# Kernel tuning notes

Hardware: AMD Instinct MI355X
Metric: run time of the kernel (lower is better)

The kernel has to match this reference:

```python
import jax, jax.numpy as jnp
import numpy as np

B, T, D_MODEL, D_STATE = 8, 2048, 1024, 256


def setup_inputs() -> dict:
    key = jax.random.key(0)
    ks = jax.random.split(key, 10)
    def lecun(k, shape):
        fan_in = shape[0]
        return jax.random.normal(k, shape, dtype=jnp.float32) / jnp.sqrt(jnp.float32(fan_in))
    return {
        "x": jax.random.normal(ks[0], (B, T, D_MODEL), dtype=jnp.float32),
        "W_in": lecun(ks[1], (D_MODEL, D_STATE)),
        "b_in": jnp.zeros((D_STATE,), dtype=jnp.float32),
        "W_gate": lecun(ks[2], (D_MODEL, D_MODEL)),
        "b_gate": jnp.zeros((D_MODEL,), dtype=jnp.float32),
        "W_out": lecun(ks[3], (D_MODEL, D_MODEL)),
        "b_out": jnp.zeros((D_MODEL,), dtype=jnp.float32),
        "A": lecun(ks[4], (D_STATE, D_STATE)) * 0.1,  # scaled for recurrence stability
        "Bm": lecun(ks[5], (D_STATE, D_STATE)),
        "C": lecun(ks[6], (D_MODEL, D_STATE)),
        "D": lecun(ks[7], (D_MODEL, D_STATE)),
    }


def reference(x, W_in, b_in, W_gate, b_gate, W_out, b_out, A, Bm, C, D):
    # Input projection to state dim and gating branch (Flax Dense: y = x @ kernel + b)
    u = x @ W_in + b_in                      # [B, T, d_state]
    gate = jax.nn.sigmoid(x @ W_gate + b_gate)  # [B, T, d_model]

    # Linear state-space recurrence: h_t = h_{t-1} @ A + u_t @ Bm
    u_t_first = jnp.swapaxes(u, 0, 1)        # [T, B, d_state]
    h0 = jnp.zeros((x.shape[0], A.shape[0]), dtype=x.dtype)

    def step(h, u_t):
        h = h @ A + u_t @ Bm
        return h, h

    _, hs = jax.lax.scan(step, h0, u_t_first)
    hs = jnp.swapaxes(hs, 0, 1)              # [B, T, d_state]

    # Readout y_t = C h_t + D u_t, gated, then output projection
    y = jnp.einsum('btn,dn->btd', hs, C) + jnp.einsum('btn,dn->btd', u, D)
    y = y * gate
    return y @ W_out + b_out
```

## Files before the change

kernel.cpp:

```cpp
#include <hip/hip_runtime.h>
#include <math.h>

#define NT 16384
#define DM 1024
#define DS 256
#define TSEQ 2048
#define KTAPS 16

typedef __bf16 bf16x8 __attribute__((ext_vector_type(8)));
typedef float f32x4 __attribute__((ext_vector_type(4)));

__device__ __forceinline__ unsigned short f2bf(float f) {
  unsigned int u = __float_as_uint(f);
  return (unsigned short)((u + 0x7FFFu + ((u >> 16) & 1u)) >> 16);
}
__device__ __forceinline__ float bf2f(unsigned short s) {
  return __uint_as_float(((unsigned int)s) << 16);
}

__device__ __forceinline__ void gload16(const void* g, void* l) {
  __builtin_amdgcn_global_load_lds(
      (const __attribute__((address_space(1))) unsigned int*)(unsigned long long)g,
      (__attribute__((address_space(3))) unsigned int*)(unsigned int)(unsigned long long)l,
      16, 0, 0);
}

__device__ __forceinline__ int xcd_swizzle(int orig, int nwg) {
  const int q = nwg >> 3, r = nwg & 7;
  const int xcd = orig & 7, idx = orig >> 3;
  return (xcd < r ? xcd * (q + 1) : r * (q + 1) + (xcd - r) * q) + idx;
}

template<int EPI, bool CONV>
__global__ __launch_bounds__(256)
void gemm128(const unsigned short* __restrict__ A, int lda,
             const unsigned short* __restrict__ Bt, int ldb,
             const float* __restrict__ bias, const float* __restrict__ bias2,
             void* Cout, int ldc, unsigned short* gatep,
             const unsigned short* __restrict__ zp, int K)
{
  __shared__ unsigned short As[3][128 * 32];
  __shared__ unsigned short Bs[3][128 * 32];
  const int tid = threadIdx.x;
  const int wave = tid >> 6, lane = tid & 63;
  const int wr = wave >> 1, wc = wave & 1;
  const int gx = gridDim.x;
  const int wg = xcd_swizzle(blockIdx.y * gx + blockIdx.x, gx * gridDim.y);
  const int row0 = (wg / gx) * 128, col0 = (wg % gx) * 128;
  const int ktiles = K >> 5;
  const int kc = CONV ? blockIdx.z : 0;

  auto stage = [&](int t, int bf) {
    const int kg = CONV ? (kc * 1024 + t * 32) : (t * 32);
    const int tap = CONV ? (kg >> 8) : 0;
    const int kin = CONV ? (kg & 255) : kg;
#pragma unroll
    for (int i = 0; i < 2; ++i) {
      const int ci = tid + i * 256;
      const int row = ci >> 2;
      const int chunk = (ci & 3) ^ ((row >> 1) & 3);
      const unsigned short* src;
      if (CONV) {
        const int r = row0 + row;
        src = ((r & (TSEQ - 1)) >= tap)
            ? A + (size_t)(r - tap) * 512 + 256 + kin + chunk * 8
            : zp + chunk * 8;
      } else {
        src = A + (size_t)(row0 + row) * lda + kin + chunk * 8;
      }
      gload16(src, &As[bf][i * 2048 + tid * 8]);
    }
#pragma unroll
    for (int i = 0; i < 2; ++i) {
      const int ci = tid + i * 256;
      const int row = ci >> 2;
      const int chunk = (ci & 3) ^ ((row >> 1) & 3);
      const unsigned short* src = CONV
          ? Bt + ((size_t)tap << 16) + (size_t)(col0 + row) * 256 + kin + chunk * 8
          : Bt + (size_t)(col0 + row) * ldb + kin + chunk * 8;
      gload16(src, &Bs[bf][i * 2048 + tid * 8]);
    }
  };

  f32x4 acc[4][4];
#pragma unroll
  for (int m = 0; m < 4; ++m)
#pragma unroll
    for (int n = 0; n < 4; ++n)
#pragma unroll
      for (int i = 0; i < 4; ++i) acc[m][n][i] = 0.f;

  const int l15 = lane & 15, lhi = lane >> 4;
  const int cs = (lhi ^ ((l15 >> 1) & 3)) * 8;
  const int aro = (wr * 64 + l15) * 32 + cs;
  const int bro = (wc * 64 + l15) * 32 + cs;

  stage(0, 0);
  stage(1, 1);
  for (int t = 0; t < ktiles; ++t) {
    const int bf = t % 3;
    if (t + 1 < ktiles) {
      asm volatile("s_waitcnt vmcnt(4)" ::: "memory");
    } else {
      asm volatile("s_waitcnt vmcnt(0)" ::: "memory");
    }
    asm volatile("s_barrier" ::: "memory");
    if (t + 2 < ktiles) stage(t + 2, (t + 2) % 3);
    bf16x8 a[4], b[4];
#pragma unroll
    for (int m = 0; m < 4; ++m) a[m] = *(const bf16x8*)(&As[bf][aro + m * 512]);
#pragma unroll
    for (int n = 0; n < 4; ++n) b[n] = *(const bf16x8*)(&Bs[bf][bro + n * 512]);
    __builtin_amdgcn_s_setprio(1);
#pragma unroll
    for (int m = 0; m < 4; ++m)
#pragma unroll
      for (int n = 0; n < 4; ++n)
        acc[m][n] = __builtin_amdgcn_mfma_f32_16x16x32_bf16(a[m], b[n], acc[m][n], 0, 0, 0);
    __builtin_amdgcn_s_setprio(0);
  }

  const int rb = row0 + wr * 64 + lhi * 4;
  const int cb = col0 + wc * 64 + l15;
#pragma unroll
  for (int m = 0; m < 4; ++m) {
#pragma unroll
    for (int n = 0; n < 4; ++n) {
      const int c = cb + n * 16;
#pragma unroll
      for (int i = 0; i < 4; ++i) {
        const size_t r = (size_t)rb + m * 16 + i;
        float v = acc[m][n][i];
        if (EPI == 2) {
          unsigned short* o = (unsigned short*)Cout;
          o[r * ldc + c] = f2bf(v * bf2f(gatep[r * ldc + c]));
        } else if (EPI == 3) {
          ((float*)Cout)[r * ldc + c] = v + bias[c];
        } else if (EPI == 4) {
          if (c < 256) {
            ((unsigned short*)Cout)[r * 512 + 256 + c] = f2bf(v + bias[c]);
          } else {
            gatep[r * 1024 + (c - 256)] = f2bf(1.f / (1.f + __expf(-(v + bias2[c - 256]))));
          }
        } else {
          ((unsigned short*)Cout)[((size_t)kc << 22) + r * 256 + c] = f2bf(v);
        }
      }
    }
  }
}

__global__ __launch_bounds__(256)
void reduce4_k(const unsigned short* __restrict__ PK, unsigned short* __restrict__ HU)
{
  const int i = blockIdx.x * 256 + threadIdx.x;
  const size_t e = (size_t)i * 4;
  const int row = i >> 6, col = (i & 63) * 4;
  float s[4] = {0.f, 0.f, 0.f, 0.f};
#pragma unroll
  for (int kc = 0; kc < 4; ++kc) {
    const ushort4 v = *(const ushort4*)(PK + ((size_t)kc << 22) + e);
    s[0] += bf2f(v.x); s[1] += bf2f(v.y); s[2] += bf2f(v.z); s[3] += bf2f(v.w);
  }
  ushort4 o;
  o.x = f2bf(s[0]); o.y = f2bf(s[1]); o.z = f2bf(s[2]); o.w = f2bf(s[3]);
  *(ushort4*)(HU + (size_t)row * 512 + col) = o;
}

__global__ __launch_bounds__(256)
void powstep(float* M, const float* Pold, float* Pnew, int nM)
{
  __shared__ float As[16][64];
  __shared__ float Bs[16][64];
  const int tid = threadIdx.x;
  const int g = blockIdx.x >> 4, sub = blockIdx.x & 15;
  const float* Ain; float* Cout;
  if (g < nM) { Ain = M + (size_t)g * 65536; Cout = M + (size_t)(nM + g) * 65536; }
  else        { Ain = Pold;                  Cout = Pnew; }
  const int row0 = (sub >> 2) * 64, col0 = (sub & 3) * 64;
  const int sar = tid >> 2, sak = (tid & 3) * 4;
  const int sbk = tid >> 4, sbc = (tid & 15) * 4;
  const int ty = tid >> 4, tx = tid & 15;
  float acc[4][4] = {};
  for (int kt = 0; kt < DS; kt += 16) {
    const float4 av = *(const float4*)(Ain + (size_t)(row0 + sar) * DS + kt + sak);
    const float4 bv = *(const float4*)(Pold + (size_t)(kt + sbk) * DS + col0 + sbc);
    __syncthreads();
    As[sak + 0][sar] = av.x; As[sak + 1][sar] = av.y;
    As[sak + 2][sar] = av.z; As[sak + 3][sar] = av.w;
    *(float4*)&Bs[sbk][sbc] = bv;
    __syncthreads();
#pragma unroll
    for (int kk = 0; kk < 16; ++kk) {
      float a[4], b[4];
      *(float4*)a = *(const float4*)&As[kk][ty * 4];
      *(float4*)b = *(const float4*)&Bs[kk][tx * 4];
#pragma unroll
      for (int i = 0; i < 4; ++i)
#pragma unroll
        for (int j = 0; j < 4; ++j) acc[i][j] = fmaf(a[i], b[j], acc[i][j]);
    }
  }
#pragma unroll
  for (int i = 0; i < 4; ++i)
    *(float4*)(Cout + (size_t)(row0 + ty * 4 + i) * DS + col0 + tx * 4) =
        make_float4(acc[i][0], acc[i][1], acc[i][2], acc[i][3]);
}

__global__ __launch_bounds__(256)
void cast_x_k(const float* __restrict__ x, unsigned short* __restrict__ xb, int n4)
{
  const int stride = gridDim.x * blockDim.x;
  for (int i = blockIdx.x * blockDim.x + threadIdx.x; i < n4; i += stride) {
    float4 v = ((const float4*)x)[i];
    ushort4 o;
    o.x = f2bf(v.x); o.y = f2bf(v.y); o.z = f2bf(v.z); o.w = f2bf(v.w);
    ((ushort4*)xb)[i] = o;
  }
}

__global__ __launch_bounds__(256)
void transpose_cast_k(const float* __restrict__ in, unsigned short* __restrict__ out,
                      int R, int C)
{
  __shared__ float t[32][33];
  const size_t bo = (size_t)blockIdx.z * R * C;
  const int c0 = blockIdx.x * 32, r0 = blockIdx.y * 32;
  const int tx = threadIdx.x & 31, ty = threadIdx.x >> 5;
#pragma unroll
  for (int i = 0; i < 32; i += 8)
    t[ty + i][tx] = in[bo + (size_t)(r0 + ty + i) * C + c0 + tx];
  __syncthreads();
#pragma unroll
  for (int i = 0; i < 32; i += 8)
    out[bo + (size_t)(c0 + ty + i) * R + r0 + tx] = f2bf(t[tx][ty + i]);
}

__global__ __launch_bounds__(256)
void transpose2_k(const float* __restrict__ in0, const float* __restrict__ in1,
                  unsigned short* __restrict__ o0, unsigned short* __restrict__ o1)
{
  __shared__ float t[32][33];
  const float* in = (blockIdx.z == 0) ? in0 : in1;
  unsigned short* out = (blockIdx.z == 0) ? o0 : o1;
  const int c0 = blockIdx.x * 32, r0 = blockIdx.y * 32;
  const int tx = threadIdx.x & 31, ty = threadIdx.x >> 5;
#pragma unroll
  for (int i = 0; i < 32; i += 8)
    t[ty + i][tx] = in[(size_t)(r0 + ty + i) * DM + c0 + tx];
  __syncthreads();
#pragma unroll
  for (int i = 0; i < 32; i += 8)
    out[(size_t)(c0 + ty + i) * DM + r0 + tx] = f2bf(t[tx][ty + i]);
}

__global__ __launch_bounds__(256)
void misc_prep_k(const float* __restrict__ Am, const float* __restrict__ Bmm,
                 const float* __restrict__ Cm, const float* __restrict__ Dm,
                 float* __restrict__ M0, float* __restrict__ P0,
                 unsigned short* __restrict__ zp, unsigned short* __restrict__ CD)
{
  const int i = blockIdx.x * 256 + threadIdx.x;
  if (i >= 65536 + 524288) return;
  if (i < 65536) {
    M0[i] = Bmm[i];
    P0[i] = Am[i];
    if (i < 1024) zp[i] = 0;
  } else {
    const int j = i - 65536;
    const int d = j >> 9, n = j & 511;
    const float v = (n < 256) ? Cm[(size_t)d * 256 + n] : Dm[(size_t)d * 256 + (n - 256)];
    CD[j] = f2bf(v);
  }
}

extern "C" void kernel_launch(void* const* d_in, const int* in_sizes, int n_in,
                              void* d_out, int out_size, void* d_ws, size_t ws_size,
                              hipStream_t stream)
{
  const float* x      = (const float*)d_in[0];
  const float* W_in   = (const float*)d_in[1];
  const float* b_in   = (const float*)d_in[2];
  const float* W_gate = (const float*)d_in[3];
  const float* b_gate = (const float*)d_in[4];
  const float* W_out  = (const float*)d_in[5];
  const float* b_out  = (const float*)d_in[6];
  const float* Am     = (const float*)d_in[7];
  const float* Bm     = (const float*)d_in[8];
  const float* Cm     = (const float*)d_in[9];
  const float* Dm     = (const float*)d_in[10];

  char* w = (char*)d_ws;
  unsigned short* xb   = (unsigned short*)(w);
  unsigned short* HU   = (unsigned short*)(w + 33554432);
  unsigned short* G    = (unsigned short*)(w + 50331648);
  unsigned short* WinT = (unsigned short*)(w + 83886080);
  unsigned short* WgT  = (unsigned short*)(w + 84410368);
  unsigned short* WoT  = (unsigned short*)(w + 86507520);
  unsigned short* CD   = (unsigned short*)(w + 88604672);
  unsigned short* MbT  = (unsigned short*)(w + 89653248);
  float*          Mf   = (float*)(w + 91750400);
  float*          P0   = (float*)(w + 95944704);
  float*          P1   = (float*)(w + 96206848);
  unsigned short* zp   = (unsigned short*)(w + 96468992);
  unsigned short* PK   = xb;
  float* out = (float*)d_out;

  cast_x_k<<<2048, 256, 0, stream>>>(x, xb, NT * DM / 4);
  transpose_cast_k<<<dim3(8, 32, 1), 256, 0, stream>>>(W_in, WinT, DM, DS);
  transpose2_k<<<dim3(32, 32, 2), 256, 0, stream>>>(W_gate, W_out, WgT, WoT);
  misc_prep_k<<<2304, 256, 0, stream>>>(Am, Bm, Cm, Dm, Mf, P0, zp, CD);
  powstep<<<32,  256, 0, stream>>>(Mf, P0, P1, 1);
  powstep<<<48,  256, 0, stream>>>(Mf, P1, P0, 2);
  powstep<<<80,  256, 0, stream>>>(Mf, P0, P1, 4);
  powstep<<<128, 256, 0, stream>>>(Mf, P1, nullptr, 8);
  transpose_cast_k<<<dim3(8, 8, 16), 256, 0, stream>>>(Mf, MbT, DS, DS);

  gemm128<4, false><<<dim3(10, 128), 256, 0, stream>>>(
      xb, DM, WinT, DM, b_in, b_gate, HU, 512, G, nullptr, 1024);
  gemm128<5, true><<<dim3(2, 128, 4), 256, 0, stream>>>(
      HU, 512, MbT, 256, nullptr, nullptr, PK, 256, nullptr, zp, 1024);
  reduce4_k<<<4096, 256, 0, stream>>>(PK, HU);
  gemm128<2, false><<<dim3(8, 128), 256, 0, stream>>>(
      HU, 512, CD, 512, nullptr, nullptr, G, 1024, G, nullptr, 512);
  gemm128<3, false><<<dim3(8, 128), 256, 0, stream>>>(
      G, DM, WoT, DM, b_out, nullptr, out, 1024, nullptr, nullptr, 1024);
}
```

Measured before the change: 306.1 us.

## Enlarge GEMM tiles to 256x256 with K=64 and double-buffered dynamic LDS

Replaces the 128x128, K=32 triple-buffered GEMM with a 256x256, K=64 tile run by 512 threads. Each wave now computes 128x64 of output, and the kernel double-buffers 128 KB of dynamic LDS using an 8-chunk XOR swizzle. The goal is more MFMA work per LDS and global byte and fewer blocks. In exchange, grids shrink to about 256-320 blocks, which risks poor CU balance and tail effects, and the large LDS footprint limits the kernel to one block per CU. The pipeline also adds a second barrier per k-step.

```diff
diff --git a/kernel.cpp b/kernel.cpp
--- a/kernel.cpp
+++ b/kernel.cpp
@@ -32,98 +32,104 @@
 }
 
 template<int EPI, bool CONV>
-__global__ __launch_bounds__(256)
-void gemm128(const unsigned short* __restrict__ A, int lda,
-             const unsigned short* __restrict__ Bt, int ldb,
-             const float* __restrict__ bias, const float* __restrict__ bias2,
-             void* Cout, int ldc, unsigned short* gatep,
-             const unsigned short* __restrict__ zp, int K)
-{
-  __shared__ unsigned short As[3][128 * 32];
-  __shared__ unsigned short Bs[3][128 * 32];
+__global__ __launch_bounds__(512, 2)
+void gemm256k64(const unsigned short* __restrict__ A, int lda,
+                const unsigned short* __restrict__ Bt, int ldb,
+                const float* __restrict__ bias, const float* __restrict__ bias2,
+                void* Cout, int ldc, unsigned short* gatep,
+                const unsigned short* __restrict__ zp, int K)
+{
+  extern __shared__ unsigned short lds[];
   const int tid = threadIdx.x;
   const int wave = tid >> 6, lane = tid & 63;
-  const int wr = wave >> 1, wc = wave & 1;
+  const int wr = wave >> 2, wc = wave & 3;
   const int gx = gridDim.x;
   const int wg = xcd_swizzle(blockIdx.y * gx + blockIdx.x, gx * gridDim.y);
-  const int row0 = (wg / gx) * 128, col0 = (wg % gx) * 128;
-  const int ktiles = K >> 5;
+  const int row0 = (wg / gx) * 256, col0 = (wg % gx) * 256;
+  const int ktiles = K >> 6;
   const int kc = CONV ? blockIdx.z : 0;
 
   auto stage = [&](int t, int bf) {
-    const int kg = CONV ? (kc * 1024 + t * 32) : (t * 32);
+    unsigned short* Ab = lds + bf * 32768;
+    unsigned short* Bb = Ab + 16384;
+    const int kg = CONV ? (kc * 1024 + t * 64) : (t * 64);
     const int tap = CONV ? (kg >> 8) : 0;
     const int kin = CONV ? (kg & 255) : kg;
 #pragma unroll
-    for (int i = 0; i < 2; ++i) {
-      const int ci = tid + i * 256;
-      const int row = ci >> 2;
-      const int chunk = (ci & 3) ^ ((row >> 1) & 3);
+    for (int i = 0; i < 4; ++i) {
+      const int ci = tid + i * 512;
+      const int row = ci >> 3;
+      const int c8 = (ci & 7) ^ (row & 7);
       const unsigned short* src;
       if (CONV) {
         const int r = row0 + row;
         src = ((r & (TSEQ - 1)) >= tap)
-            ? A + (size_t)(r - tap) * 512 + 256 + kin + chunk * 8
-            : zp + chunk * 8;
+            ? A + (size_t)(r - tap) * 512 + 256 + kin + c8 * 8
+            : zp + c8 * 8;
       } else {
-        src = A + (size_t)(row0 + row) * lda + kin + chunk * 8;
+        src = A + (size_t)(row0 + row) * lda + kin + c8 * 8;
       }
-      gload16(src, &As[bf][i * 2048 + tid * 8]);
-    }
-#pragma unroll
-    for (int i = 0; i < 2; ++i) {
-      const int ci = tid + i * 256;
-      const int row = ci >> 2;
-      const int chunk = (ci & 3) ^ ((row >> 1) & 3);
+      gload16(src, Ab + (size_t)ci * 8);
+    }
+#pragma unroll
+    for (int i = 0; i < 4; ++i) {
+      const int ci = tid + i * 512;
+      const int row = ci >> 3;
+      const int c8 = (ci & 7) ^ (row & 7);
       const unsigned short* src = CONV
-          ? Bt + ((size_t)tap << 16) + (size_t)(col0 + row) * 256 + kin + chunk * 8
-          : Bt + (size_t)(col0 + row) * ldb + kin + chunk * 8;
-      gload16(src, &Bs[bf][i * 2048 + tid * 8]);
+          ? Bt + ((size_t)tap << 16) + (size_t)(col0 + row) * 256 + kin + c8 * 8
+          : Bt + (size_t)(col0 + row) * ldb + kin + c8 * 8;
+      gload16(src, Bb + (size_t)ci * 8);
     }
   };
 
-  f32x4 acc[4][4];
-#pragma unroll
-  for (int m = 0; m < 4; ++m)
+  f32x4 acc[8][4];
+#pragma unroll
+  for (int m = 0; m < 8; ++m)
 #pragma unroll
     for (int n = 0; n < 4; ++n)
 #pragma unroll
       for (int i = 0; i < 4; ++i) acc[m][n][i] = 0.f;
 
-  const int l15 = lane & 15, lhi = lane >> 4;
-  const int cs = (lhi ^ ((l15 >> 1) & 3)) * 8;
-  const int aro = (wr * 64 + l15) * 32 + cs;
-  const int bro = (wc * 64 + l15) * 32 + cs;
+  const int l15 = lane & 15, l7 = lane & 7, lhi = lane >> 4;
+  const int aBase = (wr * 128 + l15) * 64;
+  const int bBase = (wc * 64 + l15) * 64;
 
   stage(0, 0);
-  stage(1, 1);
   for (int t = 0; t < ktiles; ++t) {
-    const int bf = t % 3;
+    const int bf = t & 1;
     if (t + 1 < ktiles) {
-      asm volatile("s_waitcnt vmcnt(4)" ::: "memory");
+      stage(t + 1, bf ^ 1);
+      asm volatile("s_waitcnt vmcnt(8)" ::: "memory");
     } else {
       asm volatile("s_waitcnt vmcnt(0)" ::: "memory");
     }
     asm volatile("s_barrier" ::: "memory");
-    if (t + 2 < ktiles) stage(t + 2, (t + 2) % 3);
-    bf16x8 a[4], b[4];
-#pragma unroll
-    for (int m = 0; m < 4; ++m) a[m] = *(const bf16x8*)(&As[bf][aro + m * 512]);
-#pragma unroll
-    for (int n = 0; n < 4; ++n) b[n] = *(const bf16x8*)(&Bs[bf][bro + n * 512]);
+    const unsigned short* Ab = lds + bf * 32768;
+    const unsigned short* Bb = Ab + 16384;
     __builtin_amdgcn_s_setprio(1);
 #pragma unroll
-    for (int m = 0; m < 4; ++m)
-#pragma unroll
-      for (int n = 0; n < 4; ++n)
-        acc[m][n] = __builtin_amdgcn_mfma_f32_16x16x32_bf16(a[m], b[n], acc[m][n], 0, 0, 0);
+    for (int kk = 0; kk < 2; ++kk) {
+      const int cs = ((kk * 4 + lhi) ^ l7) * 8;
+      bf16x8 b[4];
+#pragma unroll
+      for (int n = 0; n < 4; ++n) b[n] = *(const bf16x8*)(Bb + bBase + n * 1024 + cs);
+#pragma unroll
+      for (int m = 0; m < 8; ++m) {
+        const bf16x8 a = *(const bf16x8*)(Ab + aBase + m * 1024 + cs);
+#pragma unroll
+        for (int n = 0; n < 4; ++n)
+          acc[m][n] = __builtin_amdgcn_mfma_f32_16x16x32_bf16(a, b[n], acc[m][n], 0, 0, 0);
+      }
+    }
     __builtin_amdgcn_s_setprio(0);
-  }
-
-  const int rb = row0 + wr * 64 + lhi * 4;
+    asm volatile("s_barrier" ::: "memory");
+  }
+
+  const int rb = row0 + wr * 128 + lhi * 4;
   const int cb = col0 + wc * 64 + l15;
 #pragma unroll
-  for (int m = 0; m < 4; ++m) {
+  for (int m = 0; m < 8; ++m) {
 #pragma unroll
     for (int n = 0; n < 4; ++n) {
       const int c = cb + n * 16;
@@ -316,13 +322,14 @@
   powstep<<<128, 256, 0, stream>>>(Mf, P1, nullptr, 8);
   transpose_cast_k<<<dim3(8, 8, 16), 256, 0, stream>>>(Mf, MbT, DS, DS);
 
-  gemm128<4, false><<<dim3(10, 128), 256, 0, stream>>>(
+  const size_t LDSB = 131072;
+  gemm256k64<4, false><<<dim3(5, 64), 512, LDSB, stream>>>(
       xb, DM, WinT, DM, b_in, b_gate, HU, 512, G, nullptr, 1024);
-  gemm128<5, true><<<dim3(2, 128, 4), 256, 0, stream>>>(
+  gemm256k64<5, true><<<dim3(1, 64, 4), 512, LDSB, stream>>>(
       HU, 512, MbT, 256, nullptr, nullptr, PK, 256, nullptr, zp, 1024);
   reduce4_k<<<4096, 256, 0, stream>>>(PK, HU);
-  gemm128<2, false><<<dim3(8, 128), 256, 0, stream>>>(
+  gemm256k64<2, false><<<dim3(4, 64), 512, LDSB, stream>>>(
       HU, 512, CD, 512, nullptr, nullptr, G, 1024, G, nullptr, 512);
-  gemm128<3, false><<<dim3(8, 128), 256, 0, stream>>>(
+  gemm256k64<3, false><<<dim3(4, 64), 512, LDSB, stream>>>(
       G, DM, WoT, DM, b_out, nullptr, out, 1024, nullptr, nullptr, 1024);
 }
```

After: 323.9 us. +5.8%, slower.
